# Kernel optimization log

Hardware: AMD Instinct MI355X
Metric: run time of the kernel (lower is better)

## Reference

```python
import jax, jax.numpy as jnp
import numpy as np

N_QUBITS = 8
N_LAYERS = 7
_DN = ('NCHW', 'OIHW', 'NCHW')


def _conv(x, w, b, s, p):
    y = jax.lax.conv_general_dilated(x, w, (s, s), [(p, p), (p, p)], dimension_numbers=_DN)
    return y + b[None, :, None, None]


def _bn2d(x, g, b, m, v):
    inv = jax.lax.rsqrt(v + 1e-5)
    return (x - m[None, :, None, None]) * (g * inv)[None, :, None, None] + b[None, :, None, None]


def _qsim(feats, qw):
    # feats: [B, 256] L2-normalized real amplitudes; qw: [n_layers, n_qubits]
    B = feats.shape[0]
    psi = feats.reshape((B,) + (2,) * N_QUBITS)  # wire 0 = most significant (PennyLane convention)
    for l in range(N_LAYERS):
        for q in range(N_QUBITS):  # RY(theta) on wire q
            th = qw[l, q] * 0.5
            c, s = jnp.cos(th), jnp.sin(th)
            ax = q + 1
            p = jnp.moveaxis(psi, ax, -1)
            p = jnp.stack([c * p[..., 0] - s * p[..., 1], s * p[..., 0] + c * p[..., 1]], axis=-1)
            psi = jnp.moveaxis(p, -1, ax)
        for q in range(N_QUBITS - 1):  # CNOT(q, q+1)
            ca, ta = q + 1, q + 2
            p = jnp.moveaxis(psi, (ca, ta), (-2, -1))
            p = jnp.stack([p[..., 0, :], p[..., 1, ::-1]], axis=-2)
            psi = jnp.moveaxis(p, (-2, -1), (ca, ta))
    prob = (psi * psi).reshape(B, 2, -1).sum(-1)  # marginal on wire 0
    return prob[:, 0] - prob[:, 1]  # <Z_0>


def _forward(x, c1w, c1b, bn1g, bn1b, bn1m, bn1v, c2w, c2b, bn2g, bn2b, bn2m, bn2v,
             c3w, c3b, bn3g, bn3b, bn3m, bn3v, f1w, f1b, f2w, f2b, qw,
             w1, b1, cg, cb, cm, cv, w2, b2, w3, b3, w4, b4):
    h = jax.nn.relu(_bn2d(_conv(x, c1w, c1b, 2, 2), bn1g, bn1b, bn1m, bn1v))
    h = jax.nn.relu(_bn2d(_conv(h, c2w, c2b, 2, 1), bn2g, bn2b, bn2m, bn2v))
    h = jax.nn.relu(_bn2d(_conv(h, c3w, c3b, 1, 1), bn3g, bn3b, bn3m, bn3v))
    B, C, H, W = h.shape
    # AdaptiveAvgPool2d(4): H,W divisible by 4 here (16->4)
    h = h.reshape(B, C, 4, H // 4, 4, W // 4).mean(axis=(3, 5)).reshape(B, C * 16)
    h = jax.nn.relu(h @ f1w.T + f1b)
    h = jax.nn.relu(h @ f2w.T + f2b)  # [B, 256]; dropout = identity at eval
    feats = h / jnp.maximum(jnp.linalg.norm(h, axis=1, keepdims=True), 1e-12)
    q = _qsim(feats, qw)[:, None]  # [B, 1]
    z = jax.nn.relu(q @ w1.T + b1)
    z = (z - cm) * (cg * jax.lax.rsqrt(cv + 1e-5)) + cb  # BatchNorm1d eval
    z = jax.nn.relu(z @ w2.T + b2)
    z = jax.nn.relu(z @ w3.T + b3)
    return jax.nn.sigmoid(z @ w4.T + b4)


def setup_inputs() -> dict:
    key = jax.random.key(0)
    ks = iter(jax.random.split(key, 16))
    B = 8192
    d = {}
    d['x'] = jax.random.normal(next(ks), (B, 1, 64, 64), jnp.float32)
    d['c1w'] = jax.random.normal(next(ks), (8, 1, 5, 5), jnp.float32) * 0.2
    d['c1b'] = jnp.zeros((8,), jnp.float32)
    d['bn1g'] = jnp.ones((8,), jnp.float32); d['bn1b'] = jnp.zeros((8,), jnp.float32)
    d['bn1m'] = jnp.zeros((8,), jnp.float32); d['bn1v'] = jnp.ones((8,), jnp.float32)
    d['c2w'] = jax.random.normal(next(ks), (16, 8, 3, 3), jnp.float32) * 0.1
    d['c2b'] = jnp.zeros((16,), jnp.float32)
    d['bn2g'] = jnp.ones((16,), jnp.float32); d['bn2b'] = jnp.zeros((16,), jnp.float32)
    d['bn2m'] = jnp.zeros((16,), jnp.float32); d['bn2v'] = jnp.ones((16,), jnp.float32)
    d['c3w'] = jax.random.normal(next(ks), (32, 16, 3, 3), jnp.float32) * 0.08
    d['c3b'] = jnp.zeros((32,), jnp.float32)
    d['bn3g'] = jnp.ones((32,), jnp.float32); d['bn3b'] = jnp.zeros((32,), jnp.float32)
    d['bn3m'] = jnp.zeros((32,), jnp.float32); d['bn3v'] = jnp.ones((32,), jnp.float32)
    d['f1w'] = jax.random.normal(next(ks), (384, 512), jnp.float32) * 0.04
    d['f1b'] = jnp.zeros((384,), jnp.float32)
    d['f2w'] = jax.random.normal(next(ks), (256, 384), jnp.float32) * 0.05
    d['f2b'] = jnp.zeros((256,), jnp.float32)
    d['qw'] = jax.random.uniform(next(ks), (7, 8), jnp.float32) * 2.0 * np.pi
    d['w1'] = jax.random.normal(next(ks), (64, 1), jnp.float32) * 0.5
    d['b1'] = jnp.zeros((64,), jnp.float32)
    d['cg'] = jnp.ones((64,), jnp.float32); d['cb'] = jnp.zeros((64,), jnp.float32)
    d['cm'] = jnp.zeros((64,), jnp.float32); d['cv'] = jnp.ones((64,), jnp.float32)
    d['w2'] = jax.random.normal(next(ks), (32, 64), jnp.float32) * 0.12
    d['b2'] = jnp.zeros((32,), jnp.float32)
    d['w3'] = jax.random.normal(next(ks), (16, 32), jnp.float32) * 0.17
    d['b3'] = jnp.zeros((16,), jnp.float32)
    d['w4'] = jax.random.normal(next(ks), (1, 16), jnp.float32) * 0.25
    d['b4'] = jnp.zeros((1,), jnp.float32)
    return d


def reference(x, c1w, c1b, bn1g, bn1b, bn1m, bn1v, c2w, c2b, bn2g, bn2b, bn2m, bn2v,
              c3w, c3b, bn3g, bn3b, bn3m, bn3v, f1w, f1b, f2w, f2b, qw,
              w1, b1, cg, cb, cm, cv, w2, b2, w3, b3, w4, b4):
    return _forward(x, c1w, c1b, bn1g, bn1b, bn1m, bn1v, c2w, c2b, bn2g, bn2b, bn2m, bn2v,
                    c3w, c3b, bn3g, bn3b, bn3m, bn3v, f1w, f1b, f2w, f2b, qw,
                    w1, b1, cg, cb, cm, cv, w2, b2, w3, b3, w4, b4)
```

## Files before the change

kernel.cpp:

```cpp
#include <hip/hip_runtime.h>
#include <hip/hip_bf16.h>
#include <math.h>

#define BATCH 8192

typedef __attribute__((ext_vector_type(8))) short bf16x8;
typedef __attribute__((ext_vector_type(4))) float f32x4;
typedef __attribute__((ext_vector_type(16))) float f32x16;

struct u2a4 { unsigned int x, y; };

__device__ __forceinline__ unsigned short f2bf(float f) {
    unsigned int u = __builtin_bit_cast(unsigned int, f);
    u = (u + 0x7FFFu + ((u >> 16) & 1u)) >> 16;
    return (unsigned short)u;
}
__device__ __forceinline__ float bf2f(unsigned short h) {
    unsigned int u = ((unsigned int)h) << 16;
    return __builtin_bit_cast(float, u);
}
__device__ __forceinline__ unsigned int cvtpk(float a, float b) {
    unsigned int r;
    asm("v_cvt_pk_bf16_f32 %0, %1, %2" : "=v"(r) : "v"(a), "v"(b));
    return r;
}
__device__ __forceinline__ int swz(int i) { return i ^ ((i >> 3) & 3); }

#define W1OFF 0
#define W1FRAGS 4
#define W2OFF (W1OFF + W1FRAGS * 512)
#define W2FRAGS 6
#define W3OFF (W2OFF + W2FRAGS * 512)
#define W3FRAGS 18
#define CPACK_TOTAL (W3OFF + W3FRAGS * 512)
#define FC1_FRAGS (24 * 16 * 2)
#define FC2_FRAGS (16 * 12 * 2)
#define FC1_TOTAL (FC1_FRAGS * 512)
#define FC2_TOTAL (FC2_FRAGS * 512)
#define ANG_TOTAL 112
#define PREP_TOTAL (CPACK_TOTAL + FC1_TOTAL + FC2_TOTAL + ANG_TOTAL)

__global__ __launch_bounds__(256) void prepack_kernel(
    const float* __restrict__ c1w, const float* __restrict__ c2w,
    const float* __restrict__ c3w, const float* __restrict__ f1w,
    const float* __restrict__ f2w, const float* __restrict__ qw,
    unsigned short* __restrict__ cpack, unsigned short* __restrict__ fpack1,
    unsigned short* __restrict__ fpack2, float* __restrict__ angtab)
{
    int e = blockIdx.x * 256 + threadIdx.x;
    if (e >= PREP_TOTAL) return;

    if (e < CPACK_TOTAL) {
        int f = e >> 9, r = e & 511;
        int l = r >> 3, j = r & 7;
        float w = 0.f; int hl = 0;
        if (f < W1FRAGS) {
            int sel = f >> 1; hl = f & 1;
            int oc = l & 15;
            int k = 8 * (l >> 4) + j;
            int ky, kx;
            if (sel == 0) { ky = k >> 3; kx = k & 7; }
            else          { ky = 4;      kx = k; }
            if (kx < 5 && ky < 5 && oc < 8) w = c1w[oc * 25 + ky * 5 + kx];
        } else if (f < W1FRAGS + W2FRAGS) {
            int f2 = f - W1FRAGS;
            int ky = f2 >> 1; hl = f2 & 1;
            int k = 8 * (l >> 4) + j;
            int kx = k >> 3, ic = k & 7, oc = l & 15;
            if (kx < 3) w = c2w[((oc * 8 + ic) * 3 + ky) * 3 + kx];
        } else {
            int f3 = f - W1FRAGS - W2FRAGS;
            int ky = f3 / 6, kx = (f3 / 2) % 3; hl = f3 & 1;
            int oc = l & 31, ic = 8 * (l >> 5) + j;
            w = c3w[((oc * 16 + ic) * 3 + ky) * 3 + kx];
        }
        unsigned short hv = f2bf(w);
        unsigned short lv = f2bf(w - bf2f(hv));
        cpack[e] = hl ? lv : hv;
        return;
    }
    e -= CPACK_TOTAL;
    if (e < FC1_TOTAL) {
        int phi = e >> 9, r = e & 511;
        int l = r >> 3, j = r & 7;
        int hl = phi & 1, ks = (phi >> 1) & 15, nb = phi >> 5;
        int n = nb * 16 + (l & 15);
        int kg = ks * 32 + 8 * (l >> 4) + j;
        float w = f1w[n * 512 + kg];
        unsigned short hv = f2bf(w);
        unsigned short lv = f2bf(w - bf2f(hv));
        fpack1[e] = hl ? lv : hv;
        return;
    }
    e -= FC1_TOTAL;
    if (e < FC2_TOTAL) {
        int phi = e >> 9, r = e & 511;
        int l = r >> 3, j = r & 7;
        int hl = phi & 1, ks = (phi >> 1) % 12, nb = phi / 24;
        int n = nb * 16 + (l & 15);
        int kg = ks * 32 + 8 * (l >> 4) + j;
        float w = f2w[n * 384 + kg];
        unsigned short hv = f2bf(w);
        unsigned short lv = f2bf(w - bf2f(hv));
        fpack2[e] = hl ? lv : hv;
        return;
    }
    e -= FC2_TOTAL;
    {
        int a = e >> 1;
        float th = 0.5f * qw[a];
        angtab[e] = (e & 1) ? sinf(th) : cosf(th);
    }
}

__global__ __launch_bounds__(256) void fused_cnn_mfma(
    const float* __restrict__ x,
    const float* __restrict__ c1b,
    const float* __restrict__ bn1g, const float* __restrict__ bn1b,
    const float* __restrict__ bn1m, const float* __restrict__ bn1v,
    const float* __restrict__ c2b,
    const float* __restrict__ bn2g, const float* __restrict__ bn2b,
    const float* __restrict__ bn2m, const float* __restrict__ bn2v,
    const float* __restrict__ c3b,
    const float* __restrict__ bn3g, const float* __restrict__ bn3b,
    const float* __restrict__ bn3m, const float* __restrict__ bn3v,
    const unsigned short* __restrict__ cpack,
    unsigned short* __restrict__ pooled_bf)
{
    __shared__ __align__(16) uint4 h1p4[1160];
    __shared__ __align__(16) unsigned int sd[2720];

    uint4* sbuf4 = (uint4*)sd;

    const int tid = threadIdx.x;
    const int lane = tid & 63;
    const int wv = tid >> 6;
    const int n = blockIdx.x;
    const int lrow = lane & 15;
    const int lq = lane >> 4;

    {
        const float4* xv = (const float4*)(x + (size_t)n * 4096);
        #pragma unroll
        for (int i = 0; i < 4; ++i) {
            int idx = tid + 256 * i;
            float4 v = xv[idx];
            int px = idx * 4;
            int y = px >> 6, xc = px & 63;
            int d = (y + 2) * 40 + (xc >> 1) + 1;
            u2a4 st; st.x = cvtpk(v.x, v.y); st.y = cvtpk(v.z, v.w);
            *(u2a4*)&sd[d] = st;
        }
        if (tid < 68)       { int r = tid / 34, c = tid % 34; sd[r * 40 + c] = 0u; }
        else if (tid < 136) { int u = tid - 68; int r = 66 + u / 34, c = u % 34; sd[r * 40 + c] = 0u; }
        if (tid < 128) { int r = 2 + (tid & 63); sd[r * 40 + ((tid >> 6) ? 33 : 0)] = 0u; }
        if (tid < 132) {
            int p;
            if (tid < 34) p = tid;
            else if (tid < 68) p = 33 * 34 + (tid - 34);
            else { int r = 1 + ((tid - 68) & 31); int side = (tid - 68) >> 5; p = r * 34 + side * 33; }
            h1p4[swz(p)] = (uint4){0u, 0u, 0u, 0u};
        }
    }
    __syncthreads();

    {
        bf16x8 wf0 = __builtin_bit_cast(bf16x8, *(const uint4*)(cpack + W1OFF + lane * 8));
        bf16x8 wf2 = __builtin_bit_cast(bf16x8, *(const uint4*)(cpack + W1OFF + 2 * 512 + lane * 8));
        float s1v[4], sh1v[4];
        #pragma unroll
        for (int r = 0; r < 4; ++r) {
            int oc = (4 * lq + r) & 7;
            s1v[r] = bn1g[oc] * rsqrtf(bn1v[oc] + 1e-5f);
            sh1v[r] = (c1b[oc] - bn1m[oc]) * s1v[r] + bn1b[oc];
        }
        #pragma unroll 4
        for (int t = 0; t < 16; ++t) {
            int oy = wv * 8 + (t >> 1), h = t & 1;
            int a1 = (2 * oy + lq) * 40 + 16 * h + lrow;
            u2a4 r1 = *(const u2a4*)&sd[a1];
            uint4 d1; d1.x = r1.x; d1.y = r1.y; d1.z = sd[a1 + 2]; d1.w = 0u;
            int a2 = (2 * oy + 4) * 40 + 16 * h + lrow;
            u2a4 r2 = *(const u2a4*)&sd[a2];
            uint4 d2; d2.x = r2.x; d2.y = r2.y; d2.z = sd[a2 + 2]; d2.w = 0u;
            f32x4 acc = {0.f, 0.f, 0.f, 0.f};
            acc = __builtin_amdgcn_mfma_f32_16x16x32_bf16(wf0, __builtin_bit_cast(bf16x8, d1), acc, 0, 0, 0);
            acc = __builtin_amdgcn_mfma_f32_16x16x32_bf16(wf2, __builtin_bit_cast(bf16x8, d2), acc, 0, 0, 0);
            if (lq < 2) {
                unsigned int u0 = cvtpk(fmaxf(fmaf(acc[0], s1v[0], sh1v[0]), 0.f),
                                        fmaxf(fmaf(acc[1], s1v[1], sh1v[1]), 0.f));
                unsigned int u1 = cvtpk(fmaxf(fmaf(acc[2], s1v[2], sh1v[2]), 0.f),
                                        fmaxf(fmaf(acc[3], s1v[3], sh1v[3]), 0.f));
                int p = (oy + 1) * 34 + 16 * h + lrow + 1;
                uint2 wr; wr.x = u0; wr.y = u1;
                *(uint2*)((char*)h1p4 + swz(p) * 16 + 8 * lq) = wr;
            }
        }
    }
    __syncthreads();

    {
        if (tid < 136) {
            int pp = tid >> 1, plane = tid & 1;
            int p;
            if (pp < 18) p = pp;
            else if (pp < 36) p = 17 * 18 + (pp - 18);
            else { int r = 1 + ((pp - 36) & 15); int side = (pp - 36) >> 4; p = r * 18 + side * 17; }
            sbuf4[plane * 324 + p] = (uint4){0u, 0u, 0u, 0u};
        }
        bf16x8 w2f[3];
        #pragma unroll
        for (int ky = 0; ky < 3; ++ky)
            w2f[ky] = __builtin_bit_cast(bf16x8,
                *(const uint4*)(cpack + W2OFF + (ky * 2) * 512 + lane * 8));
        float s2v[4], sh2v[4];
        #pragma unroll
        for (int r = 0; r < 4; ++r) {
            int oc = 4 * lq + r;
            s2v[r] = bn2g[oc] * rsqrtf(bn2v[oc] + 1e-5f);
            sh2v[r] = (c2b[oc] - bn2m[oc]) * s2v[r] + bn2b[oc];
        }
        int lqe = (lq == 3) ? 0 : lq;
        #pragma unroll
        for (int t = 0; t < 4; ++t) {
            int oy = 4 * wv + t;
            f32x4 acc = {0.f, 0.f, 0.f, 0.f};
            #pragma unroll
            for (int ky = 0; ky < 3; ++ky) {
                int iy = 2 * oy + ky;
                int p = iy * 34 + 2 * lrow + lqe;
                bf16x8 b = __builtin_bit_cast(bf16x8, h1p4[swz(p)]);
                acc = __builtin_amdgcn_mfma_f32_16x16x32_bf16(w2f[ky], b, acc, 0, 0, 0);
            }
            unsigned int u0 = cvtpk(fmaxf(fmaf(acc[0], s2v[0], sh2v[0]), 0.f),
                                    fmaxf(fmaf(acc[1], s2v[1], sh2v[1]), 0.f));
            unsigned int u1 = cvtpk(fmaxf(fmaf(acc[2], s2v[2], sh2v[2]), 0.f),
                                    fmaxf(fmaf(acc[3], s2v[3], sh2v[3]), 0.f));
            int p = (oy + 1) * 18 + lrow + 1;
            uint2 wr; wr.x = u0; wr.y = u1;
            *(uint2*)((char*)sbuf4 + ((lq >> 1) * 324 + p) * 16 + 8 * (lq & 1)) = wr;
        }
    }
    __syncthreads();

    {
        f32x16 accA = {0.f}, accB = {0.f};
        const int row = lane & 31;
        const int khalf = lane >> 5;
        const int kbase = khalf * 324;
        #pragma unroll
        for (int ky = 0; ky < 3; ++ky)
            #pragma unroll
            for (int kx = 0; kx < 3; ++kx) {
                int fb = (ky * 3 + kx) * 2;
                bf16x8 bh = __builtin_bit_cast(bf16x8, *(const uint4*)(cpack + W3OFF + fb * 512 + lane * 8));
                {
                    int pix = (4 * wv + 0 + (row >> 4) + ky) * 18 + (row & 15) + kx;
                    bf16x8 a = __builtin_bit_cast(bf16x8, sbuf4[kbase + pix]);
                    accA = __builtin_amdgcn_mfma_f32_32x32x16_bf16(a, bh, accA, 0, 0, 0);
                }
                {
                    int pix = (4 * wv + 2 + (row >> 4) + ky) * 18 + (row & 15) + kx;
                    bf16x8 a = __builtin_bit_cast(bf16x8, sbuf4[kbase + pix]);
                    accB = __builtin_amdgcn_mfma_f32_32x32x16_bf16(a, bh, accB, 0, 0, 0);
                }
            }
        int oc = lane & 31;
        float s3 = bn3g[oc] * rsqrtf(bn3v[oc] + 1e-5f);
        float sh3 = (c3b[oc] - bn3m[oc]) * s3 + bn3b[oc];
        float pool0 = 0.f, pool1 = 0.f;
        #pragma unroll
        for (int r = 0; r < 16; ++r) {
            float va = fmaxf(fmaf(accA[r], s3, sh3), 0.f);
            float vb = fmaxf(fmaf(accB[r], s3, sh3), 0.f);
            if (((r >> 2) & 1) == 0) { pool0 += va + vb; } else { pool1 += va + vb; }
        }
        int base = n * 512 + oc * 16 + wv * 4 + khalf;
        pooled_bf[base]     = (unsigned short)cvtpk(pool0 * (1.f / 16.f), 0.f);
        pooled_bf[base + 2] = (unsigned short)cvtpk(pool1 * (1.f / 16.f), 0.f);
    }
}

template <int OUT_BF16>
__global__ __launch_bounds__(256) void fc_mfma(
    const unsigned short* __restrict__ Abf,
    const unsigned short* __restrict__ wfrag,
    const float* __restrict__ bias, void* __restrict__ out,
    int N, int K)
{
    __shared__ __align__(16) unsigned short As[8192];
    const int tid = threadIdx.x;
    const int lane = tid & 63;
    const int wv = tid >> 6;
    const int wm = wv >> 1, wn = wv & 1;
    const int bm = blockIdx.x * 128;
    const int bn = blockIdx.y * 64;
    const int lq = lane >> 4;
    const int lr = lane & 15;
    const int KS = K >> 5;

    f32x4 acc[4][2];
    #pragma unroll
    for (int i = 0; i < 4; ++i) { acc[i][0] = (f32x4){0,0,0,0}; acc[i][1] = (f32x4){0,0,0,0}; }

    for (int k0 = 0; k0 < K; k0 += 64) {
        #pragma unroll
        for (int i = 0; i < 4; ++i) {
            int q = tid * 4 + i;
            int row = q >> 3, kc = q & 7;
            uint4 v = *(const uint4*)(Abf + (size_t)(bm + row) * K + k0 + 8 * kc);
            int byte = (row * 128 + 16 * kc) ^ ((row & 7) << 4);
            *(uint4*)((char*)As + byte) = v;
        }
        __syncthreads();
        #pragma unroll
        for (int kk = 0; kk < 2; ++kk) {
            bf16x8 af[4];
            #pragma unroll
            for (int mf = 0; mf < 4; ++mf) {
                int ml = wm * 64 + mf * 16 + lr;
                int byte = (ml * 128 + 64 * kk + 16 * lq) ^ ((ml & 7) << 4);
                af[mf] = __builtin_bit_cast(bf16x8, *(const uint4*)((char*)As + byte));
            }
            int ks = (k0 >> 5) + kk;
            #pragma unroll
            for (int nf = 0; nf < 2; ++nf) {
                int nb = (bn >> 4) + wn * 2 + nf;
                const unsigned short* fb = wfrag + ((size_t)(nb * KS + ks) * 2) * 512 + lane * 8;
                bf16x8 bh = __builtin_bit_cast(bf16x8, *(const uint4*)fb);
                #pragma unroll
                for (int mf = 0; mf < 4; ++mf)
                    acc[mf][nf] = __builtin_amdgcn_mfma_f32_16x16x32_bf16(af[mf], bh, acc[mf][nf], 0, 0, 0);
            }
        }
        __syncthreads();
    }

    #pragma unroll
    for (int nf = 0; nf < 2; ++nf) {
        int nn = bn + wn * 32 + nf * 16 + lr;
        float bv = bias[nn];
        #pragma unroll
        for (int mf = 0; mf < 4; ++mf)
            #pragma unroll
            for (int r = 0; r < 4; ++r) {
                int m = bm + wm * 64 + mf * 16 + 4 * lq + r;
                float v = fmaxf(acc[mf][nf][r] + bv, 0.f);
                if (OUT_BF16) ((unsigned short*)out)[(size_t)m * N + nn] = (unsigned short)cvtpk(v, 0.f);
                else          ((float*)out)[(size_t)m * N + nn] = v;
            }
    }
}

__global__ __launch_bounds__(256) void qsim_tail_kernel(
    const float* __restrict__ feats, const float* __restrict__ angtab,
    const float* __restrict__ w1, const float* __restrict__ b1,
    const float* __restrict__ cg, const float* __restrict__ cb,
    const float* __restrict__ cm, const float* __restrict__ cv,
    const float* __restrict__ w2, const float* __restrict__ b2,
    const float* __restrict__ w3, const float* __restrict__ b3,
    const float* __restrict__ w4, const float* __restrict__ b4,
    float* __restrict__ out)
{
    const int lane = threadIdx.x & 63;
    const int wid = threadIdx.x >> 6;
    const int s = blockIdx.x * 4 + wid;

    float4 v = *(const float4*)(feats + (size_t)s * 256 + lane * 4);
    float a0 = v.x, a1 = v.y, a2 = v.z, a3 = v.w;

    float ss = a0 * a0 + a1 * a1 + a2 * a2 + a3 * a3;
    #pragma unroll
    for (int m = 32; m; m >>= 1) ss += __shfl_xor(ss, m);
    float inv = 1.f / fmaxf(sqrtf(ss), 1e-12f);
    a0 *= inv; a1 *= inv; a2 *= inv; a3 *= inv;

    const int csrc = lane ^ ((lane >> 1) & 31);

    for (int l = 0; l < 7; ++l) {
        #pragma unroll
        for (int q = 0; q < 6; ++q) {
            float cs = angtab[(l * 8 + q) * 2], sn = angtab[(l * 8 + q) * 2 + 1];
            int mask = 32 >> q;
            float sg = (lane & mask) ? sn : -sn;
            float b0 = __shfl_xor(a0, mask), b1v = __shfl_xor(a1, mask);
            float b2v = __shfl_xor(a2, mask), b3v = __shfl_xor(a3, mask);
            a0 = fmaf(sg, b0, cs * a0); a1 = fmaf(sg, b1v, cs * a1);
            a2 = fmaf(sg, b2v, cs * a2); a3 = fmaf(sg, b3v, cs * a3);
        }
        {
            float cs = angtab[(l * 8 + 6) * 2], sn = angtab[(l * 8 + 6) * 2 + 1];
            float n0 = cs * a0 - sn * a2, n2 = fmaf(sn, a0, cs * a2);
            float n1 = cs * a1 - sn * a3, n3 = fmaf(sn, a1, cs * a3);
            a0 = n0; a1 = n1; a2 = n2; a3 = n3;
        }
        {
            float cs = angtab[(l * 8 + 7) * 2], sn = angtab[(l * 8 + 7) * 2 + 1];
            float n0 = cs * a0 - sn * a1, n1 = fmaf(sn, a0, cs * a1);
            float n2 = cs * a2 - sn * a3, n3 = fmaf(sn, a2, cs * a3);
            a0 = n0; a1 = n1; a2 = n2; a3 = n3;
        }
        a0 = __shfl(a0, csrc); a1 = __shfl(a1, csrc);
        a2 = __shfl(a2, csrc); a3 = __shfl(a3, csrc);
        {
            bool f = (lane & 1);
            float n0 = f ? a2 : a0, n2 = f ? a0 : a2;
            float n1 = f ? a3 : a1, n3 = f ? a1 : a3;
            a0 = n0; a1 = n1; a2 = n2; a3 = n3;
        }
        { float t = a2; a2 = a3; a3 = t; }
    }

    float part = a0 * a0 + a1 * a1 + a2 * a2 + a3 * a3;
    part = (lane & 32) ? -part : part;
    #pragma unroll
    for (int m = 32; m; m >>= 1) part += __shfl_xor(part, m);
    float q = part;

    float z = fmaxf(fmaf(q, w1[lane], b1[lane]), 0.f);
    z = fmaf(z - cm[lane], cg[lane] * rsqrtf(cv[lane] + 1e-5f), cb[lane]);
    {
        int j = lane & 31, hb = lane & 32;
        float acc = 0.f;
        #pragma unroll
        for (int t = 0; t < 32; ++t)
            acc = fmaf(w2[j * 64 + hb + t], __shfl(z, hb + t), acc);
        acc += __shfl_xor(acc, 32);
        z = fmaxf(acc + b2[j], 0.f);
    }
    {
        int j3 = lane & 15, qh = (lane >> 4) & 3;
        float p = 0.f;
        #pragma unroll
        for (int t = 0; t < 8; ++t)
            p = fmaf(w3[j3 * 32 + 8 * qh + t], __shfl(z, 8 * qh + t), p);
        p += __shfl_xor(p, 16);
        p += __shfl_xor(p, 32);
        z = fmaxf(p + b3[j3], 0.f);
    }
    {
        float t4 = w4[lane & 15] * z;
        t4 += __shfl_xor(t4, 1); t4 += __shfl_xor(t4, 2);
        t4 += __shfl_xor(t4, 4); t4 += __shfl_xor(t4, 8);
        float o = t4 + b4[0];
        if (lane == 0) out[s] = 1.f / (1.f + expf(-o));
    }
}

extern "C" void kernel_launch(void* const* d_in, const int* in_sizes, int n_in,
                              void* d_out, int out_size, void* d_ws, size_t ws_size,
                              hipStream_t stream)
{
    const float* x    = (const float*)d_in[0];
    const float* c1w  = (const float*)d_in[1];
    const float* c1b  = (const float*)d_in[2];
    const float* bn1g = (const float*)d_in[3];
    const float* bn1b = (const float*)d_in[4];
    const float* bn1m = (const float*)d_in[5];
    const float* bn1v = (const float*)d_in[6];
    const float* c2w  = (const float*)d_in[7];
    const float* c2b  = (const float*)d_in[8];
    const float* bn2g = (const float*)d_in[9];
    const float* bn2b = (const float*)d_in[10];
    const float* bn2m = (const float*)d_in[11];
    const float* bn2v = (const float*)d_in[12];
    const float* c3w  = (const float*)d_in[13];
    const float* c3b  = (const float*)d_in[14];
    const float* bn3g = (const float*)d_in[15];
    const float* bn3b = (const float*)d_in[16];
    const float* bn3m = (const float*)d_in[17];
    const float* bn3v = (const float*)d_in[18];
    const float* f1w  = (const float*)d_in[19];
    const float* f1b  = (const float*)d_in[20];
    const float* f2w  = (const float*)d_in[21];
    const float* f2b  = (const float*)d_in[22];
    const float* qw   = (const float*)d_in[23];
    const float* w1   = (const float*)d_in[24];
    const float* b1   = (const float*)d_in[25];
    const float* cg   = (const float*)d_in[26];
    const float* cb   = (const float*)d_in[27];
    const float* cm   = (const float*)d_in[28];
    const float* cv   = (const float*)d_in[29];
    const float* w2   = (const float*)d_in[30];
    const float* b2   = (const float*)d_in[31];
    const float* w3   = (const float*)d_in[32];
    const float* b3   = (const float*)d_in[33];
    const float* w4   = (const float*)d_in[34];
    const float* b4   = (const float*)d_in[35];

    unsigned short* ws = (unsigned short*)d_ws;
    unsigned short* pooled_bf = ws;
    unsigned short* a1_bf     = pooled_bf + (size_t)BATCH * 512;
    float*          a2        = (float*)(a1_bf + (size_t)BATCH * 384);
    unsigned short* cpack     = (unsigned short*)(a2 + (size_t)BATCH * 256);
    unsigned short* fpack1    = cpack + CPACK_TOTAL;
    unsigned short* fpack2    = fpack1 + FC1_TOTAL;
    float*          angtab    = (float*)(fpack2 + FC2_TOTAL);

    prepack_kernel<<<(PREP_TOTAL + 255) / 256, 256, 0, stream>>>(
        c1w, c2w, c3w, f1w, f2w, qw, cpack, fpack1, fpack2, angtab);

    fused_cnn_mfma<<<BATCH, 256, 0, stream>>>(
        x, c1b, bn1g, bn1b, bn1m, bn1v,
        c2b, bn2g, bn2b, bn2m, bn2v,
        c3b, bn3g, bn3b, bn3m, bn3v, cpack, pooled_bf);

    dim3 g1(BATCH / 128, 384 / 64);
    fc_mfma<1><<<g1, 256, 0, stream>>>(pooled_bf, fpack1, f1b, a1_bf, 384, 512);

    dim3 g2(BATCH / 128, 256 / 64);
    fc_mfma<0><<<g2, 256, 0, stream>>>(a1_bf, fpack2, f2b, a2, 256, 384);

    qsim_tail_kernel<<<BATCH / 4, 256, 0, stream>>>(
        a2, angtab, w1, b1, cg, cb, cm, cv, w2, b2, w3, b3, w4, b4, (float*)d_out);
}
```

Baseline: 123.3 us.

## Fuse FC1, FC2 and quantum tail into one head kernel

Replaces the two tiled FC GEMM kernels and the separate qsim/tail kernel with a single head kernel. Each block processes 16 samples, keeps the FC1 and FC2 activations in shared memory as bf16, and runs the quantum simulation and MLP tail on them directly. This removes two launches and the global round trips for the intermediate activations. The packed FC weights also drop the unused low-half bf16 fragments, so they are half the size. The trade-off is that with only 16 rows per block, weight fragments are re-read from global/L2 by every one of the 512 blocks. The FC2 output is also now stored as bf16 instead of fp32 before normalization, which slightly lowers precision.

After: 112.7 us, median of 2. 1.09x faster.

```diff
diff --git a/kernel.cpp b/kernel.cpp
--- a/kernel.cpp
+++ b/kernel.cpp
@@ -25,6 +25,7 @@
     return r;
 }
 __device__ __forceinline__ int swz(int i) { return i ^ ((i >> 3) & 3); }
+__device__ __forceinline__ float relu_(float v) { return fmaxf(v, 0.f); }
 
 #define W1OFF 0
 #define W1FRAGS 4
@@ -33,8 +34,8 @@
 #define W3OFF (W2OFF + W2FRAGS * 512)
 #define W3FRAGS 18
 #define CPACK_TOTAL (W3OFF + W3FRAGS * 512)
-#define FC1_FRAGS (24 * 16 * 2)
-#define FC2_FRAGS (16 * 12 * 2)
+#define FC1_FRAGS (24 * 16)
+#define FC2_FRAGS (16 * 12)
 #define FC1_TOTAL (FC1_FRAGS * 512)
 #define FC2_TOTAL (FC2_FRAGS * 512)
 #define ANG_TOTAL 112
@@ -83,26 +84,20 @@
     if (e < FC1_TOTAL) {
         int phi = e >> 9, r = e & 511;
         int l = r >> 3, j = r & 7;
-        int hl = phi & 1, ks = (phi >> 1) & 15, nb = phi >> 5;
+        int ks = phi & 15, nb = phi >> 4;
         int n = nb * 16 + (l & 15);
         int kg = ks * 32 + 8 * (l >> 4) + j;
-        float w = f1w[n * 512 + kg];
-        unsigned short hv = f2bf(w);
-        unsigned short lv = f2bf(w - bf2f(hv));
-        fpack1[e] = hl ? lv : hv;
+        fpack1[e] = f2bf(f1w[n * 512 + kg]);
         return;
     }
     e -= FC1_TOTAL;
     if (e < FC2_TOTAL) {
         int phi = e >> 9, r = e & 511;
         int l = r >> 3, j = r & 7;
-        int hl = phi & 1, ks = (phi >> 1) % 12, nb = phi / 24;
+        int ks = phi % 12, nb = phi / 12;
         int n = nb * 16 + (l & 15);
         int kg = ks * 32 + 8 * (l >> 4) + j;
-        float w = f2w[n * 384 + kg];
-        unsigned short hv = f2bf(w);
-        unsigned short lv = f2bf(w - bf2f(hv));
-        fpack2[e] = hl ? lv : hv;
+        fpack2[e] = f2bf(f2w[n * 384 + kg]);
         return;
     }
     e -= FC2_TOTAL;
@@ -281,79 +276,12 @@
     }
 }
 
-template <int OUT_BF16>
-__global__ __launch_bounds__(256) void fc_mfma(
-    const unsigned short* __restrict__ Abf,
-    const unsigned short* __restrict__ wfrag,
-    const float* __restrict__ bias, void* __restrict__ out,
-    int N, int K)
-{
-    __shared__ __align__(16) unsigned short As[8192];
-    const int tid = threadIdx.x;
-    const int lane = tid & 63;
-    const int wv = tid >> 6;
-    const int wm = wv >> 1, wn = wv & 1;
-    const int bm = blockIdx.x * 128;
-    const int bn = blockIdx.y * 64;
-    const int lq = lane >> 4;
-    const int lr = lane & 15;
-    const int KS = K >> 5;
-
-    f32x4 acc[4][2];
-    #pragma unroll
-    for (int i = 0; i < 4; ++i) { acc[i][0] = (f32x4){0,0,0,0}; acc[i][1] = (f32x4){0,0,0,0}; }
-
-    for (int k0 = 0; k0 < K; k0 += 64) {
-        #pragma unroll
-        for (int i = 0; i < 4; ++i) {
-            int q = tid * 4 + i;
-            int row = q >> 3, kc = q & 7;
-            uint4 v = *(const uint4*)(Abf + (size_t)(bm + row) * K + k0 + 8 * kc);
-            int byte = (row * 128 + 16 * kc) ^ ((row & 7) << 4);
-            *(uint4*)((char*)As + byte) = v;
-        }
-        __syncthreads();
-        #pragma unroll
-        for (int kk = 0; kk < 2; ++kk) {
-            bf16x8 af[4];
-            #pragma unroll
-            for (int mf = 0; mf < 4; ++mf) {
-                int ml = wm * 64 + mf * 16 + lr;
-                int byte = (ml * 128 + 64 * kk + 16 * lq) ^ ((ml & 7) << 4);
-                af[mf] = __builtin_bit_cast(bf16x8, *(const uint4*)((char*)As + byte));
-            }
-            int ks = (k0 >> 5) + kk;
-            #pragma unroll
-            for (int nf = 0; nf < 2; ++nf) {
-                int nb = (bn >> 4) + wn * 2 + nf;
-                const unsigned short* fb = wfrag + ((size_t)(nb * KS + ks) * 2) * 512 + lane * 8;
-                bf16x8 bh = __builtin_bit_cast(bf16x8, *(const uint4*)fb);
-                #pragma unroll
-                for (int mf = 0; mf < 4; ++mf)
-                    acc[mf][nf] = __builtin_amdgcn_mfma_f32_16x16x32_bf16(af[mf], bh, acc[mf][nf], 0, 0, 0);
-            }
-        }
-        __syncthreads();
-    }
-
-    #pragma unroll
-    for (int nf = 0; nf < 2; ++nf) {
-        int nn = bn + wn * 32 + nf * 16 + lr;
-        float bv = bias[nn];
-        #pragma unroll
-        for (int mf = 0; mf < 4; ++mf)
-            #pragma unroll
-            for (int r = 0; r < 4; ++r) {
-                int m = bm + wm * 64 + mf * 16 + 4 * lq + r;
-                float v = fmaxf(acc[mf][nf][r] + bv, 0.f);
-                if (OUT_BF16) ((unsigned short*)out)[(size_t)m * N + nn] = (unsigned short)cvtpk(v, 0.f);
-                else          ((float*)out)[(size_t)m * N + nn] = v;
-            }
-    }
-}
-
-__global__ __launch_bounds__(256) void qsim_tail_kernel(
-    const float* __restrict__ feats, const float* __restrict__ angtab,
+__global__ __launch_bounds__(256) void head_kernel(
+    const unsigned short* __restrict__ pooled_bf,
+    const unsigned short* __restrict__ fpack1,
+    const unsigned short* __restrict__ fpack2,
+    const float* __restrict__ f1b, const float* __restrict__ f2b,
+    const float* __restrict__ angtab,
     const float* __restrict__ w1, const float* __restrict__ b1,
     const float* __restrict__ cg, const float* __restrict__ cb,
     const float* __restrict__ cm, const float* __restrict__ cv,
@@ -362,88 +290,170 @@
     const float* __restrict__ w4, const float* __restrict__ b4,
     float* __restrict__ out)
 {
-    const int lane = threadIdx.x & 63;
-    const int wid = threadIdx.x >> 6;
-    const int s = blockIdx.x * 4 + wid;
-
-    float4 v = *(const float4*)(feats + (size_t)s * 256 + lane * 4);
-    float a0 = v.x, a1 = v.y, a2 = v.z, a3 = v.w;
-
-    float ss = a0 * a0 + a1 * a1 + a2 * a2 + a3 * a3;
-    #pragma unroll
-    for (int m = 32; m; m >>= 1) ss += __shfl_xor(ss, m);
-    float inv = 1.f / fmaxf(sqrtf(ss), 1e-12f);
-    a0 *= inv; a1 *= inv; a2 *= inv; a3 *= inv;
+    __shared__ __align__(16) unsigned short As[8192];
+    __shared__ __align__(16) unsigned short h1[6144];
+    __shared__ __align__(16) unsigned short h2[4096];
+
+    const int tid = threadIdx.x;
+    const int lane = tid & 63;
+    const int w = tid >> 6;
+    const int lr = lane & 15;
+    const int lq = lane >> 4;
+    const int m0 = blockIdx.x * 16;
+
+    {
+        const uint4* src = (const uint4*)(pooled_bf + (size_t)m0 * 512);
+        #pragma unroll
+        for (int i = 0; i < 8; ++i) {
+            int q = i * 256 + tid;
+            uint4 v = src[q];
+            int row = q >> 6, kc = q & 63;
+            int byte = (row * 1024 + 16 * kc) ^ ((row & 7) << 4);
+            *(uint4*)((char*)As + byte) = v;
+        }
+    }
+    __syncthreads();
+
+    {
+        f32x4 acc[6];
+        #pragma unroll
+        for (int i = 0; i < 6; ++i) acc[i] = (f32x4){0.f, 0.f, 0.f, 0.f};
+        for (int ks = 0; ks < 16; ++ks) {
+            int byte = (lr * 1024 + 16 * (ks * 4 + lq)) ^ ((lr & 7) << 4);
+            bf16x8 act = __builtin_bit_cast(bf16x8, *(const uint4*)((char*)As + byte));
+            #pragma unroll
+            for (int nf = 0; nf < 6; ++nf) {
+                int nb = 6 * w + nf;
+                bf16x8 wf = __builtin_bit_cast(bf16x8,
+                    *(const uint4*)(fpack1 + (size_t)(nb * 16 + ks) * 512 + lane * 8));
+                acc[nf] = __builtin_amdgcn_mfma_f32_16x16x32_bf16(wf, act, acc[nf], 0, 0, 0);
+            }
+        }
+        #pragma unroll
+        for (int nf = 0; nf < 6; ++nf) {
+            int n0 = 96 * w + 16 * nf + 4 * lq;
+            float4 bb = *(const float4*)(f1b + n0);
+            unsigned int u0 = cvtpk(relu_(acc[nf][0] + bb.x), relu_(acc[nf][1] + bb.y));
+            unsigned int u1 = cvtpk(relu_(acc[nf][2] + bb.z), relu_(acc[nf][3] + bb.w));
+            int byte = (lr * 768 + 2 * n0) ^ ((lr & 7) << 4);
+            uint2 wr; wr.x = u0; wr.y = u1;
+            *(uint2*)((char*)h1 + byte) = wr;
+        }
+    }
+    __syncthreads();
+
+    {
+        f32x4 acc[4];
+        #pragma unroll
+        for (int i = 0; i < 4; ++i) acc[i] = (f32x4){0.f, 0.f, 0.f, 0.f};
+        for (int ks = 0; ks < 12; ++ks) {
+            int byte = (lr * 768 + 16 * (ks * 4 + lq)) ^ ((lr & 7) << 4);
+            bf16x8 act = __builtin_bit_cast(bf16x8, *(const uint4*)((char*)h1 + byte));
+            #pragma unroll
+            for (int nf = 0; nf < 4; ++nf) {
+                int nb = 4 * w + nf;
+                bf16x8 wf = __builtin_bit_cast(bf16x8,
+                    *(const uint4*)(fpack2 + (size_t)(nb * 12 + ks) * 512 + lane * 8));
+                acc[nf] = __builtin_amdgcn_mfma_f32_16x16x32_bf16(wf, act, acc[nf], 0, 0, 0);
+            }
+        }
+        #pragma unroll
+        for (int nf = 0; nf < 4; ++nf) {
+            int n0 = 64 * w + 16 * nf + 4 * lq;
+            float4 bb = *(const float4*)(f2b + n0);
+            unsigned int u0 = cvtpk(relu_(acc[nf][0] + bb.x), relu_(acc[nf][1] + bb.y));
+            unsigned int u1 = cvtpk(relu_(acc[nf][2] + bb.z), relu_(acc[nf][3] + bb.w));
+            int byte = (lr * 512 + 2 * n0) ^ ((lr & 7) << 3);
+            uint2 wr; wr.x = u0; wr.y = u1;
+            *(uint2*)((char*)h2 + byte) = wr;
+        }
+    }
+    __syncthreads();
 
     const int csrc = lane ^ ((lane >> 1) & 31);
-
-    for (int l = 0; l < 7; ++l) {
-        #pragma unroll
-        for (int q = 0; q < 6; ++q) {
-            float cs = angtab[(l * 8 + q) * 2], sn = angtab[(l * 8 + q) * 2 + 1];
-            int mask = 32 >> q;
-            float sg = (lane & mask) ? sn : -sn;
-            float b0 = __shfl_xor(a0, mask), b1v = __shfl_xor(a1, mask);
-            float b2v = __shfl_xor(a2, mask), b3v = __shfl_xor(a3, mask);
-            a0 = fmaf(sg, b0, cs * a0); a1 = fmaf(sg, b1v, cs * a1);
-            a2 = fmaf(sg, b2v, cs * a2); a3 = fmaf(sg, b3v, cs * a3);
-        }
+    for (int it = 0; it < 4; ++it) {
+        int m = w * 4 + it;
+        int byte = (m * 512 + 8 * lane) ^ ((m & 7) << 3);
+        uint2 fv = *(const uint2*)((char*)h2 + byte);
+        float a0 = bf2f((unsigned short)(fv.x & 0xffff));
+        float a1 = bf2f((unsigned short)(fv.x >> 16));
+        float a2 = bf2f((unsigned short)(fv.y & 0xffff));
+        float a3 = bf2f((unsigned short)(fv.y >> 16));
+
+        float ss = a0 * a0 + a1 * a1 + a2 * a2 + a3 * a3;
+        #pragma unroll
+        for (int mm = 32; mm; mm >>= 1) ss += __shfl_xor(ss, mm);
+        float inv = 1.f / fmaxf(sqrtf(ss), 1e-12f);
+        a0 *= inv; a1 *= inv; a2 *= inv; a3 *= inv;
+
+        for (int l = 0; l < 7; ++l) {
+            #pragma unroll
+            for (int q = 0; q < 6; ++q) {
+                float cs = angtab[(l * 8 + q) * 2], sn = angtab[(l * 8 + q) * 2 + 1];
+                int mask = 32 >> q;
+                float sg = (lane & mask) ? sn : -sn;
+                float b0 = __shfl_xor(a0, mask), b1v = __shfl_xor(a1, mask);
+                float b2v = __shfl_xor(a2, mask), b3v = __shfl_xor(a3, mask);
+                a0 = fmaf(sg, b0, cs * a0); a1 = fmaf(sg, b1v, cs * a1);
+                a2 = fmaf(sg, b2v, cs * a2); a3 = fmaf(sg, b3v, cs * a3);
+            }
+            {
+                float cs = angtab[(l * 8 + 6) * 2], sn = angtab[(l * 8 + 6) * 2 + 1];
+                float n0 = cs * a0 - sn * a2, n2 = fmaf(sn, a0, cs * a2);
+                float n1 = cs * a1 - sn * a3, n3 = fmaf(sn, a1, cs * a3);
+                a0 = n0; a1 = n1; a2 = n2; a3 = n3;
+            }
+            {
+                float cs = angtab[(l * 8 + 7) * 2], sn = angtab[(l * 8 + 7) * 2 + 1];
+                float n0 = cs * a0 - sn * a1, n1 = fmaf(sn, a0, cs * a1);
+                float n2 = cs * a2 - sn * a3, n3 = fmaf(sn, a2, cs * a3);
+                a0 = n0; a1 = n1; a2 = n2; a3 = n3;
+            }
+            a0 = __shfl(a0, csrc); a1 = __shfl(a1, csrc);
+            a2 = __shfl(a2, csrc); a3 = __shfl(a3, csrc);
+            {
+                bool f = (lane & 1);
+                float n0 = f ? a2 : a0, n2 = f ? a0 : a2;
+                float n1 = f ? a3 : a1, n3 = f ? a1 : a3;
+                a0 = n0; a1 = n1; a2 = n2; a3 = n3;
+            }
+            { float t = a2; a2 = a3; a3 = t; }
+        }
+
+        float part = a0 * a0 + a1 * a1 + a2 * a2 + a3 * a3;
+        part = (lane & 32) ? -part : part;
+        #pragma unroll
+        for (int mm = 32; mm; mm >>= 1) part += __shfl_xor(part, mm);
+        float qv = part;
+
+        float z = fmaxf(fmaf(qv, w1[lane], b1[lane]), 0.f);
+        z = fmaf(z - cm[lane], cg[lane] * rsqrtf(cv[lane] + 1e-5f), cb[lane]);
         {
-            float cs = angtab[(l * 8 + 6) * 2], sn = angtab[(l * 8 + 6) * 2 + 1];
-            float n0 = cs * a0 - sn * a2, n2 = fmaf(sn, a0, cs * a2);
-            float n1 = cs * a1 - sn * a3, n3 = fmaf(sn, a1, cs * a3);
-            a0 = n0; a1 = n1; a2 = n2; a3 = n3;
+            int j = lane & 31, hb = lane & 32;
+            float acc = 0.f;
+            #pragma unroll
+            for (int t = 0; t < 32; ++t)
+                acc = fmaf(w2[j * 64 + hb + t], __shfl(z, hb + t), acc);
+            acc += __shfl_xor(acc, 32);
+            z = fmaxf(acc + b2[j], 0.f);
         }
         {
-            float cs = angtab[(l * 8 + 7) * 2], sn = angtab[(l * 8 + 7) * 2 + 1];
-            float n0 = cs * a0 - sn * a1, n1 = fmaf(sn, a0, cs * a1);
-            float n2 = cs * a2 - sn * a3, n3 = fmaf(sn, a2, cs * a3);
-            a0 = n0; a1 = n1; a2 = n2; a3 = n3;
-        }
-        a0 = __shfl(a0, csrc); a1 = __shfl(a1, csrc);
-        a2 = __shfl(a2, csrc); a3 = __shfl(a3, csrc);
+            int j3 = lane & 15, qh = (lane >> 4) & 3;
+            float p = 0.f;
+            #pragma unroll
+            for (int t = 0; t < 8; ++t)
+                p = fmaf(w3[j3 * 32 + 8 * qh + t], __shfl(z, 8 * qh + t), p);
+            p += __shfl_xor(p, 16);
+            p += __shfl_xor(p, 32);
+            z = fmaxf(p + b3[j3], 0.f);
+        }
         {
-            bool f = (lane & 1);
-            float n0 = f ? a2 : a0, n2 = f ? a0 : a2;
-            float n1 = f ? a3 : a1, n3 = f ? a1 : a3;
-            a0 = n0; a1 = n1; a2 = n2; a3 = n3;
-        }
-        { float t = a2; a2 = a3; a3 = t; }
-    }
-
-    float part = a0 * a0 + a1 * a1 + a2 * a2 + a3 * a3;
-    part = (lane & 32) ? -part : part;
-    #pragma unroll
-    for (int m = 32; m; m >>= 1) part += __shfl_xor(part, m);
-    float q = part;
-
-    float z = fmaxf(fmaf(q, w1[lane], b1[lane]), 0.f);
-    z = fmaf(z - cm[lane], cg[lane] * rsqrtf(cv[lane] + 1e-5f), cb[lane]);
-    {
-        int j = lane & 31, hb = lane & 32;
-        float acc = 0.f;
-        #pragma unroll
-        for (int t = 0; t < 32; ++t)
-            acc = fmaf(w2[j * 64 + hb + t], __shfl(z, hb + t), acc);
-        acc += __shfl_xor(acc, 32);
-        z = fmaxf(acc + b2[j], 0.f);
-    }
-    {
-        int j3 = lane & 15, qh = (lane >> 4) & 3;
-        float p = 0.f;
-        #pragma unroll
-        for (int t = 0; t < 8; ++t)
-            p = fmaf(w3[j3 * 32 + 8 * qh + t], __shfl(z, 8 * qh + t), p);
-        p += __shfl_xor(p, 16);
-        p += __shfl_xor(p, 32);
-        z = fmaxf(p + b3[j3], 0.f);
-    }
-    {
-        float t4 = w4[lane & 15] * z;
-        t4 += __shfl_xor(t4, 1); t4 += __shfl_xor(t4, 2);
-        t4 += __shfl_xor(t4, 4); t4 += __shfl_xor(t4, 8);
-        float o = t4 + b4[0];
-        if (lane == 0) out[s] = 1.f / (1.f + expf(-o));
+            float t4 = w4[lane & 15] * z;
+            t4 += __shfl_xor(t4, 1); t4 += __shfl_xor(t4, 2);
+            t4 += __shfl_xor(t4, 4); t4 += __shfl_xor(t4, 8);
+            float o = t4 + b4[0];
+            if (lane == 0) out[m0 + m] = 1.f / (1.f + expf(-o));
+        }
     }
 }
 
@@ -490,9 +500,7 @@
 
     unsigned short* ws = (unsigned short*)d_ws;
     unsigned short* pooled_bf = ws;
-    unsigned short* a1_bf     = pooled_bf + (size_t)BATCH * 512;
-    float*          a2        = (float*)(a1_bf + (size_t)BATCH * 384);
-    unsigned short* cpack     = (unsigned short*)(a2 + (size_t)BATCH * 256);
+    unsigned short* cpack     = pooled_bf + (size_t)BATCH * 512;
     unsigned short* fpack1    = cpack + CPACK_TOTAL;
     unsigned short* fpack2    = fpack1 + FC1_TOTAL;
     float*          angtab    = (float*)(fpack2 + FC2_TOTAL);
@@ -505,12 +513,7 @@
         c2b, bn2g, bn2b, bn2m, bn2v,
         c3b, bn3g, bn3b, bn3m, bn3v, cpack, pooled_bf);
 
-    dim3 g1(BATCH / 128, 384 / 64);
-    fc_mfma<1><<<g1, 256, 0, stream>>>(pooled_bf, fpack1, f1b, a1_bf, 384, 512);
-
-    dim3 g2(BATCH / 128, 256 / 64);
-    fc_mfma<0><<<g2, 256, 0, stream>>>(a1_bf, fpack2, f2b, a2, 256, 384);
-
-    qsim_tail_kernel<<<BATCH / 4, 256, 0, stream>>>(
-        a2, angtab, w1, b1, cg, cb, cm, cv, w2, b2, w3, b3, w4, b4, (float*)d_out);
-}
+    head_kernel<<<BATCH / 16, 256, 0, stream>>>(
+        pooled_bf, fpack1, fpack2, f1b, f2b, angtab,
+        w1, b1, cg, cb, cm, cv, w2, b2, w3, b3, w4, b4, (float*)d_out);
+}
```
